# Performance work log

Measured on AMD Instinct MI355X. Metric: run time of the kernel, lower is better.

Reference implementation:

```python
import jax, jax.numpy as jnp
import numpy as np

B, T, N_EMBD = 4, 2048, 1024
NUM_EXPERTS, TOP_K = 8, 2
N_CITIES = 4
LIN = N_EMBD + 32 + N_EMBD // 4 + N_EMBD // 4 + N_EMBD // 8 + N_EMBD // 8  # 1824


def setup_inputs() -> dict:
    key = jax.random.key(0)
    ks = jax.random.split(key, 12)
    s = 0.02  # init std as in _init_weights
    return {
        "x": jax.random.normal(ks[0], (B, T, N_EMBD), jnp.float32),
        "delta_t_info": jax.random.normal(ks[1], (B, T, N_EMBD // 4), jnp.float32),
        "delta_dis_info": jax.random.normal(ks[2], (B, T, N_EMBD // 4), jnp.float32),
        "delta_rg_info": jax.random.normal(ks[3], (B, T, N_EMBD // 8), jnp.float32),
        "delta_entropy_info": jax.random.normal(ks[4], (B, T, N_EMBD // 8), jnp.float32),
        "city_embeddings": jax.random.normal(ks[5], (N_CITIES, 32), jnp.float32),
        "Wg": jax.random.normal(ks[6], (LIN, NUM_EXPERTS), jnp.float32) * s,
        "bg": jnp.zeros((NUM_EXPERTS,), jnp.float32),
        "W1": jax.random.normal(ks[7], (NUM_EXPERTS, N_EMBD, 4 * N_EMBD), jnp.float32) * s,
        "b1": jnp.zeros((NUM_EXPERTS, 4 * N_EMBD), jnp.float32),
        "W2": jax.random.normal(ks[8], (NUM_EXPERTS, 4 * N_EMBD, N_EMBD), jnp.float32) * s,
        "b2": jnp.zeros((NUM_EXPERTS, N_EMBD), jnp.float32),
        "city_index": 1,
    }


def _moe(x, dt, dd, drg, de, city_embeddings, Wg, bg, W1, b1, W2, b2, city_index):
    b, t, _ = x.shape
    city = jnp.broadcast_to(city_embeddings[city_index], (b, t, 32))
    feats = jnp.concatenate([x, city, dt, dd, drg, de], axis=-1)  # [B,T,LIN]
    logits = jnp.einsum("btl,le->bte", feats, Wg) + bg            # eval mode: no noise
    gate1 = jax.nn.softmax(logits, axis=-1)
    _, topi = jax.lax.top_k(logits, TOP_K)                        # [B,T,k]
    # mask of top-k experts per token; scatter(-inf elsewhere) + softmax
    mask = jax.nn.one_hot(topi, NUM_EXPERTS, dtype=jnp.float32).sum(axis=-2) > 0
    sparse_logits = jnp.where(mask, logits, -jnp.inf)
    gates = jax.nn.softmax(sparse_logits, axis=-1)                # zeros outside top-k
    out = jnp.zeros_like(x)
    for e in range(NUM_EXPERTS):  # fixed small expert set
        h = jax.nn.gelu(jnp.einsum("btc,ch->bth", x, W1[e]) + b1[e], approximate=True)
        y = jnp.einsum("bth,hc->btc", h, W2[e]) + b2[e]
        out = out + gates[..., e:e + 1] * y  # gate is exactly 0 for non-topk tokens
    return out, gate1


def reference(x, delta_t_info, delta_dis_info, delta_rg_info, delta_entropy_info,
              city_embeddings, Wg, bg, W1, b1, W2, b2, city_index):
    return _moe(x, delta_t_info, delta_dis_info, delta_rg_info, delta_entropy_info,
                city_embeddings, Wg, bg, W1, b1, W2, b2, city_index)
```

## Files before the change

### kernel.cpp

```cpp
#include <hip/hip_runtime.h>
#include <hip/hip_bf16.h>
#include <stdint.h>

#define NTOK 8192
#define DEMB 1024
#define HDIM 4096
#define NEXP 8
#define LINF 1824
#define MAXPAD 18432

typedef __attribute__((ext_vector_type(8))) __bf16 bf16x8;
typedef __attribute__((ext_vector_type(4))) __bf16 bf16x4v;
typedef __attribute__((ext_vector_type(4))) float f32x4;

__device__ __forceinline__ void gload_lds16(const void* g, void* l) {
  __builtin_amdgcn_global_load_lds(
      (const __attribute__((address_space(1))) void*)g,
      (__attribute__((address_space(3))) void*)l, 16, 0, 0);
}

__device__ __forceinline__ float dot4(float4 a, float4 b) {
  return a.x*b.x + a.y*b.y + a.z*b.z + a.w*b.w;
}

__global__ void __launch_bounds__(256) k_logits(
    const float* __restrict__ x, const float* __restrict__ dt,
    const float* __restrict__ dd, const float* __restrict__ drg,
    const float* __restrict__ de, const float* __restrict__ city,
    const float* __restrict__ Wg, const float* __restrict__ bg,
    const int* __restrict__ city_index,
    float* __restrict__ gate1, int* __restrict__ top_i, float2* __restrict__ top_g,
    __bf16* __restrict__ xb)
{
  __shared__ float WgT[NEXP * LINF];
  const int tid = threadIdx.x;
  const float4* Wg4 = (const float4*)Wg;
  for (int i = tid; i < LINF * NEXP / 4; i += 256) {
    float4 v = Wg4[i];
    int e0 = (i & 1) * 4, f = i >> 1;
    WgT[(e0+0)*LINF + f] = v.x; WgT[(e0+1)*LINF + f] = v.y;
    WgT[(e0+2)*LINF + f] = v.z; WgT[(e0+3)*LINF + f] = v.w;
  }
  __syncthreads();

  const int wave = tid >> 6, lane = tid & 63;
  const int ci = city_index[0];
  const float4* city4 = (const float4*)(city + ci*32);
  const float4 z4 = {0.f, 0.f, 0.f, 0.f};

  #pragma unroll
  for (int k = 0; k < 4; ++k) {
    const int t = blockIdx.x*16 + wave*4 + k;
    const float4* x4 = (const float4*)x + (size_t)t*256;
    float4 xv0 = x4[lane], xv1 = x4[64+lane], xv2 = x4[128+lane], xv3 = x4[192+lane];

    {
      bf16x4v* xrow = (bf16x4v*)(xb + (size_t)t*1024);
      bf16x4v o0, o1, o2, o3;
      o0[0]=(__bf16)xv0.x; o0[1]=(__bf16)xv0.y; o0[2]=(__bf16)xv0.z; o0[3]=(__bf16)xv0.w;
      o1[0]=(__bf16)xv1.x; o1[1]=(__bf16)xv1.y; o1[2]=(__bf16)xv1.z; o1[3]=(__bf16)xv1.w;
      o2[0]=(__bf16)xv2.x; o2[1]=(__bf16)xv2.y; o2[2]=(__bf16)xv2.z; o2[3]=(__bf16)xv2.w;
      o3[0]=(__bf16)xv3.x; o3[1]=(__bf16)xv3.y; o3[2]=(__bf16)xv3.z; o3[3]=(__bf16)xv3.w;
      xrow[lane] = o0; xrow[64+lane] = o1; xrow[128+lane] = o2; xrow[192+lane] = o3;
    }

    float4 cv = (lane < 8) ? city4[lane] : z4;
    float4 tv = ((const float4*)dt)[(size_t)t*64 + lane];
    float4 dv = ((const float4*)dd)[(size_t)t*64 + lane];
    float4 rv = z4, ev = z4;
    if (lane < 32) {
      rv = ((const float4*)drg)[(size_t)t*32 + lane];
      ev = ((const float4*)de )[(size_t)t*32 + lane];
    }
    float a[8];
    const int l8 = lane & 7, l32 = lane & 31;
    #pragma unroll
    for (int e = 0; e < 8; ++e) {
      const float4* W = (const float4*)(WgT + e*LINF);
      float s = dot4(xv0, W[lane]) + dot4(xv1, W[64+lane])
              + dot4(xv2, W[128+lane]) + dot4(xv3, W[192+lane]);
      s += dot4(cv, W[256 + l8]);
      s += dot4(tv, W[264 + lane]) + dot4(dv, W[328 + lane]);
      s += dot4(rv, W[392 + l32]) + dot4(ev, W[424 + l32]);
      a[e] = s;
    }
    #pragma unroll
    for (int off = 32; off > 0; off >>= 1)
      #pragma unroll
      for (int e = 0; e < 8; ++e) a[e] += __shfl_xor(a[e], off);

    float lg[8];
    #pragma unroll
    for (int e = 0; e < 8; ++e) lg[e] = a[e] + bg[e];
    float mx = lg[0];
    #pragma unroll
    for (int e = 1; e < 8; ++e) mx = fmaxf(mx, lg[e]);
    float ex[8]; float s = 0.f;
    #pragma unroll
    for (int e = 0; e < 8; ++e) { ex[e] = expf(lg[e] - mx); s += ex[e]; }
    int i1 = 0; float l1 = lg[0];
    #pragma unroll
    for (int e = 1; e < 8; ++e) if (lg[e] > l1) { l1 = lg[e]; i1 = e; }
    int i2 = -1; float l2 = -1e30f;
    #pragma unroll
    for (int e = 0; e < 8; ++e) if (e != i1 && lg[e] > l2) { l2 = lg[e]; i2 = e; }
    float e2 = expf(l2 - l1);

    if (lane == 0) {
      float inv = 1.f / s;
      float4 o0 = { ex[0]*inv, ex[1]*inv, ex[2]*inv, ex[3]*inv };
      float4 o1 = { ex[4]*inv, ex[5]*inv, ex[6]*inv, ex[7]*inv };
      float4* gp = (float4*)(gate1 + (size_t)t*8);
      gp[0] = o0; gp[1] = o1;
      top_i[t] = i1 | (i2 << 4);
      float2 g = { 1.f / (1.f + e2), e2 / (1.f + e2) };
      top_g[t] = g;
    }
  }
}

__global__ void __launch_bounds__(256) k_build(
    const int* __restrict__ top_i, const float2* __restrict__ top_g,
    int* __restrict__ counts, int* __restrict__ ex_tok, float* __restrict__ ex_gate,
    int2* __restrict__ ppos)
{
  __shared__ int lcnt[8], lbase[8];
  const int tid = threadIdx.x;
  if (tid < 8) lcnt[tid] = 0;
  __syncthreads();
  const int t = blockIdx.x*256 + tid;
  const int ti = top_i[t];
  const int i1 = ti & 15, i2 = ti >> 4;
  const float2 g = top_g[t];
  int p1 = atomicAdd(&lcnt[i1], 1);
  int p2 = atomicAdd(&lcnt[i2], 1);
  __syncthreads();
  if (tid < 8) lbase[tid] = atomicAdd(&counts[tid], lcnt[tid]);
  __syncthreads();
  int s1 = lbase[i1] + p1; ex_tok[i1*NTOK+s1] = t; ex_gate[i1*NTOK+s1] = g.x;
  int s2 = lbase[i2] + p2; ex_tok[i2*NTOK+s2] = t; ex_gate[i2*NTOK+s2] = g.y;
  int2 pp = { i1 | (s1 << 3), i2 | (s2 << 3) };
  ppos[t] = pp;
}

__global__ void k_finalize(const int* __restrict__ counts, int* __restrict__ seg) {
  if (threadIdx.x == 0 && blockIdx.x == 0) {
    int s = 0;
    for (int e = 0; e < 8; ++e) { seg[e] = s; s += (counts[e] + 255) & ~255; }
    seg[8] = s;
  }
}

template<int RDIM, int CDIM>
__global__ void __launch_bounds__(256) k_tconv(
    const float* __restrict__ W, __bf16* __restrict__ WT)
{
  const int e  = blockIdx.z;
  const int c0 = blockIdx.x * 64, r0 = blockIdx.y * 64;
  __shared__ float tb[64 * 65];
  const float* src = W  + (size_t)e * RDIM * CDIM + (size_t)r0 * CDIM + c0;
  __bf16*      dst = WT + (size_t)e * RDIM * CDIM + (size_t)c0 * RDIM + r0;
  const int tx = threadIdx.x & 15, ty = threadIdx.x >> 4;
  #pragma unroll
  for (int i = 0; i < 4; ++i) {
    int r = ty + i*16;
    float4 v = *(const float4*)(src + (size_t)r*CDIM + tx*4);
    tb[(tx*4+0)*65 + r] = v.x; tb[(tx*4+1)*65 + r] = v.y;
    tb[(tx*4+2)*65 + r] = v.z; tb[(tx*4+3)*65 + r] = v.w;
  }
  __syncthreads();
  const int sg = threadIdx.x & 7, dr8 = threadIdx.x >> 3;
  #pragma unroll
  for (int i = 0; i < 2; ++i) {
    int d = dr8 + i*32;
    const float* row = tb + d*65 + sg*8;
    bf16x8 o;
    #pragma unroll
    for (int j = 0; j < 8; ++j) o[j] = (__bf16)row[j];
    *(bf16x8*)(dst + (size_t)d*RDIM + sg*8) = o;
  }
}

template<int KDIM, int KFULL, int NDIM, bool G1>
__global__ void __launch_bounds__(512, 2) k_moe_gemm8(
    const __bf16* __restrict__ Abase, const __bf16* __restrict__ WT,
    const float* __restrict__ bias,
    const int* __restrict__ seg, const int* __restrict__ counts,
    const int* __restrict__ ex_tok,
    int chunk0, __bf16* __restrict__ dstbuf)
{
  constexpr int NT = KDIM / 64;
  const int nx = gridDim.x, ny = gridDim.y, nz = gridDim.z;
  const int total = nx * ny * nz;
  int flat;
  if (G1) flat = blockIdx.x + nx * blockIdx.y;
  else    flat = blockIdx.y + ny * (blockIdx.x + nx * blockIdx.z);
  { int q = total >> 3, r = total & 7; int xcd = flat & 7, idx = flat >> 3;
    flat = (xcd < r ? xcd*(q+1) : r*(q+1) + (xcd-r)*q) + idx; }
  int bx, by, bz;
  if (G1) { bx = flat % nx; by = flat / nx; bz = 0; }
  else    { by = flat % ny; int f2 = flat / ny; bx = f2 % nx; bz = f2 / nx; }

  const int segtot = seg[8];
  const int row0 = chunk0 + bx * 256;
  if (row0 >= segtot) return;
  int e = 0;
  #pragma unroll
  for (int qq = 1; qq < 8; ++qq) if (row0 >= seg[qq]) e = qq;
  const int cnt = counts[e], sege = seg[e];
  const int n0 = by * 256;
  const int kbase = bz * KDIM;

  __shared__ __align__(16) char smem[131072];

  const int tid = threadIdx.x;
  const int wid = tid >> 6, lane = tid & 63;
  const int wm = wid >> 2, wn = wid & 3;
  const int l15 = lane & 15, l4 = lane >> 4;
  const __bf16* Bsrc = WT + (size_t)e * NDIM * KFULL;

  float bv[4];
  if (G1) {
    #pragma unroll
    for (int N = 0; N < 4; ++N)
      bv[N] = bias[(size_t)e*NDIM + n0 + wn*64 + N*16 + l15];
    asm volatile("" :: "v"(bv[0]), "v"(bv[1]), "v"(bv[2]), "v"(bv[3]));
  }

  const __bf16* sp[4][2];
  #pragma unroll
  for (int j = 0; j < 2; ++j) {
    int g = j*512 + tid;
    int sl = g >> 3;
    int kb = (g & 7) ^ (sl & 7);
    #pragma unroll
    for (int mh = 0; mh < 2; ++mh) {
      int wms = (sl >> 6) & 1, rs = sl & 63;
      int R = wms*128 + mh*64 + rs;
      int arow;
      if (G1) { int lr = row0 + R - sege; arow = (lr < cnt) ? ex_tok[e*NTOK + lr] : 0; }
      else    { arow = row0 + R - chunk0; }
      sp[mh][j] = Abase + (size_t)arow * KFULL + kbase + kb*8;
    }
    #pragma unroll
    for (int nh = 0; nh < 2; ++nh) {
      int wns = (sl >> 5) & 3, rs = sl & 31;
      int C = wns*64 + nh*32 + rs;
      sp[2+nh][j] = Bsrc + (size_t)(n0 + C) * KFULL + kbase + kb*8;
    }
  }

  int xo[2];
  #pragma unroll
  for (int kk = 0; kk < 2; ++kk) xo[kk] = (((kk*4 + l4) ^ (l15 & 7)) * 16);
  int arb[4], brb[2];
  #pragma unroll
  for (int m = 0; m < 4; ++m) arb[m] = (wm*64 + m*16 + l15) * 128;
  #pragma unroll
  for (int n = 0; n < 2; ++n) brb[n] = 32768 + (wn*32 + n*16 + l15) * 128;

  auto ISSUE = [&](int h, int tt) {
    char* b = smem + (tt & 1) * 65536 + h * 16384;
    gload_lds16(sp[h][0] + tt*64, b + tid*16);
    gload_lds16(sp[h][1] + tt*64, b + 8192 + tid*16);
  };

  f32x4 acc[8][4] = {};

  ISSUE(0,0); ISSUE(2,0); ISSUE(3,0); ISSUE(1,0);
  ISSUE(0,1); ISSUE(2,1); ISSUE(3,1);
  asm volatile("s_waitcnt vmcnt(10)" ::: "memory");
  __builtin_amdgcn_s_barrier();

  for (int t = 0; t < NT; ++t) {
    const char* cb = smem + (t & 1) * 65536;
    const int tc1 = (t+1 < NT) ? t+1 : NT-1;
    const int tc2 = (t+2 < NT) ? t+2 : NT-1;
    bf16x8 af[4][2], bfr[2][2][2];

    #pragma unroll
    for (int m = 0; m < 4; ++m)
      #pragma unroll
      for (int kk = 0; kk < 2; ++kk)
        af[m][kk] = *(const bf16x8*)(cb + arb[m] + xo[kk]);
    #pragma unroll
    for (int n = 0; n < 2; ++n)
      #pragma unroll
      for (int kk = 0; kk < 2; ++kk)
        bfr[0][n][kk] = *(const bf16x8*)(cb + brb[n] + xo[kk]);
    ISSUE(1, tc1);
    __builtin_amdgcn_s_barrier();
    asm volatile("s_waitcnt lgkmcnt(0)" ::: "memory");
    __builtin_amdgcn_sched_barrier(0);
    __builtin_amdgcn_s_setprio(1);
    #pragma unroll
    for (int m = 0; m < 4; ++m)
      #pragma unroll
      for (int n = 0; n < 2; ++n)
        #pragma unroll
        for (int kk = 0; kk < 2; ++kk)
          acc[m][n] = __builtin_amdgcn_mfma_f32_16x16x32_bf16(af[m][kk], bfr[0][n][kk], acc[m][n], 0, 0, 0);
    __builtin_amdgcn_s_setprio(0);
    asm volatile("s_waitcnt vmcnt(10)" ::: "memory");
    __builtin_amdgcn_s_barrier();

    #pragma unroll
    for (int n = 0; n < 2; ++n)
      #pragma unroll
      for (int kk = 0; kk < 2; ++kk)
        bfr[1][n][kk] = *(const bf16x8*)(cb + 16384 + brb[n] + xo[kk]);
    ISSUE(0, tc2);
    __builtin_amdgcn_s_barrier();
    asm volatile("s_waitcnt lgkmcnt(0)" ::: "memory");
    __builtin_amdgcn_sched_barrier(0);
    __builtin_amdgcn_s_setprio(1);
    #pragma unroll
    for (int m = 0; m < 4; ++m)
      #pragma unroll
      for (int n = 0; n < 2; ++n)
        #pragma unroll
        for (int kk = 0; kk < 2; ++kk)
          acc[m][2+n] = __builtin_amdgcn_mfma_f32_16x16x32_bf16(af[m][kk], bfr[1][n][kk], acc[m][2+n], 0, 0, 0);
    __builtin_amdgcn_s_setprio(0);
    asm volatile("s_waitcnt vmcnt(10)" ::: "memory");
    __builtin_amdgcn_s_barrier();

    #pragma unroll
    for (int m = 0; m < 4; ++m)
      #pragma unroll
      for (int kk = 0; kk < 2; ++kk)
        af[m][kk] = *(const bf16x8*)(cb + 16384 + arb[m] + xo[kk]);
    ISSUE(2, tc2);
    __builtin_amdgcn_s_barrier();
    asm volatile("s_waitcnt lgkmcnt(0)" ::: "memory");
    __builtin_amdgcn_sched_barrier(0);
    __builtin_amdgcn_s_setprio(1);
    #pragma unroll
    for (int m = 0; m < 4; ++m)
      #pragma unroll
      for (int n = 0; n < 2; ++n)
        #pragma unroll
        for (int kk = 0; kk < 2; ++kk)
          acc[4+m][n] = __builtin_amdgcn_mfma_f32_16x16x32_bf16(af[m][kk], bfr[0][n][kk], acc[4+m][n], 0, 0, 0);
    __builtin_amdgcn_s_setprio(0);
    asm volatile("s_waitcnt vmcnt(10)" ::: "memory");
    __builtin_amdgcn_s_barrier();

    ISSUE(3, tc2);
    __builtin_amdgcn_s_barrier();
    __builtin_amdgcn_s_setprio(1);
    #pragma unroll
    for (int m = 0; m < 4; ++m)
      #pragma unroll
      for (int n = 0; n < 2; ++n)
        #pragma unroll
        for (int kk = 0; kk < 2; ++kk)
          acc[4+m][2+n] = __builtin_amdgcn_mfma_f32_16x16x32_bf16(af[m][kk], bfr[1][n][kk], acc[4+m][2+n], 0, 0, 0);
    __builtin_amdgcn_s_setprio(0);
    asm volatile("s_waitcnt vmcnt(10)" ::: "memory");
    __builtin_amdgcn_s_barrier();
  }

  __syncthreads();
  __bf16* Cl = (__bf16*)smem;
  #pragma unroll
  for (int M = 0; M < 8; ++M) {
    #pragma unroll
    for (int N = 0; N < 4; ++N) {
      #pragma unroll
      for (int r2 = 0; r2 < 4; ++r2) {
        float v = acc[M][N][r2];
        if (G1) {
          v += bv[N];
          float z = 2.302208f * (v + 0.044715f * v * v * v);
          v = v / (1.f + exp2f(-z));
        }
        Cl[(wm*128 + M*16 + l4*4 + r2)*256 + wn*64 + N*16 + l15] = (__bf16)v;
      }
    }
  }
  __syncthreads();
  const int drow0 = G1 ? (row0 - chunk0) : row0;
  __bf16* dst = dstbuf + (G1 ? (size_t)0 : (size_t)bz * MAXPAD * NDIM);
  #pragma unroll
  for (int it = 0; it < 16; ++it) {
    int idx2 = it*512 + tid;
    int rr = idx2 >> 5, c8 = (idx2 & 31) * 8;
    *(bf16x8*)(dst + (size_t)(drow0 + rr)*NDIM + n0 + c8) =
        *(const bf16x8*)(Cl + rr*256 + c8);
  }
}

__global__ void __launch_bounds__(256) k_combine(
    const __bf16* __restrict__ pbuf, const int2* __restrict__ ppos,
    const float2* __restrict__ top_g, const int* __restrict__ seg,
    const float* __restrict__ b2, float* __restrict__ out)
{
  const int t = blockIdx.x, tid = threadIdx.x;
  const int2 pp = ppos[t];
  const float2 g = top_g[t];
  const int e1 = pp.x & 7, i1 = pp.x >> 3;
  const int e2 = pp.y & 7, i2 = pp.y >> 3;
  const size_t r1 = (size_t)(seg[e1] + i1) * DEMB;
  const size_t r2 = (size_t)(seg[e2] + i2) * DEMB;
  const __bf16* p0 = pbuf;
  const __bf16* p1 = pbuf + (size_t)MAXPAD * DEMB;
  const int c = tid * 4;
  bf16x4v a0 = *(const bf16x4v*)(p0 + r1 + c);
  bf16x4v a1 = *(const bf16x4v*)(p1 + r1 + c);
  bf16x4v c0 = *(const bf16x4v*)(p0 + r2 + c);
  bf16x4v c1 = *(const bf16x4v*)(p1 + r2 + c);
  float4 ba = *(const float4*)(b2 + (size_t)e1*DEMB + c);
  float4 bb = *(const float4*)(b2 + (size_t)e2*DEMB + c);
  float4 o;
  o.x = g.x*((float)a0[0]+(float)a1[0]+ba.x) + g.y*((float)c0[0]+(float)c1[0]+bb.x);
  o.y = g.x*((float)a0[1]+(float)a1[1]+ba.y) + g.y*((float)c0[1]+(float)c1[1]+bb.y);
  o.z = g.x*((float)a0[2]+(float)a1[2]+ba.z) + g.y*((float)c0[2]+(float)c1[2]+bb.z);
  o.w = g.x*((float)a0[3]+(float)a1[3]+ba.w) + g.y*((float)c0[3]+(float)c1[3]+bb.w);
  *(float4*)(out + (size_t)t*DEMB + c) = o;
}

extern "C" void kernel_launch(void* const* d_in, const int* in_sizes, int n_in,
                              void* d_out, int out_size, void* d_ws, size_t ws_size,
                              hipStream_t stream)
{
  const float* x   = (const float*)d_in[0];
  const float* dt  = (const float*)d_in[1];
  const float* dd  = (const float*)d_in[2];
  const float* drg = (const float*)d_in[3];
  const float* de  = (const float*)d_in[4];
  const float* city= (const float*)d_in[5];
  const float* Wg  = (const float*)d_in[6];
  const float* bg  = (const float*)d_in[7];
  const float* W1  = (const float*)d_in[8];
  const float* b1  = (const float*)d_in[9];
  const float* W2  = (const float*)d_in[10];
  const float* b2  = (const float*)d_in[11];
  const int* city_index = (const int*)d_in[12];

  float* out   = (float*)d_out;
  float* gate1 = out + (size_t)NTOK * DEMB;

  char* p = (char*)d_ws;
  int*    counts  = (int*)p;      p += 256;
  int*    seg     = (int*)p;      p += 256;
  int*    top_i   = (int*)p;      p += (size_t)NTOK*4;
  float2* top_g   = (float2*)p;   p += (size_t)NTOK*8;
  int2*   ppos    = (int2*)p;     p += (size_t)NTOK*8;
  int*    ex_tok  = (int*)p;      p += (size_t)NTOK*NEXP*4;
  float*  ex_gate = (float*)p;    p += (size_t)NTOK*NEXP*4;
  __bf16* xb      = (__bf16*)p;   p += (size_t)NTOK*DEMB*2;
  __bf16* W1T     = (__bf16*)p;   p += (size_t)NEXP*DEMB*HDIM*2;
  __bf16* W2T     = (__bf16*)p;   p += (size_t)NEXP*DEMB*HDIM*2;
  __bf16* pbuf    = (__bf16*)p;   p += (size_t)2*MAXPAD*DEMB*2;
  __bf16* hbuf    = (__bf16*)p;

  size_t fixed = (size_t)(p - (char*)d_ws);
  int CH = MAXPAD;
  while (CH > 0 && fixed + (size_t)CH * HDIM * 2 > ws_size) CH -= 256;
  if (CH <= 0) return;
  int nch = (MAXPAD + CH - 1) / CH;

  (void)hipMemsetAsync(counts, 0, 64, stream);

  k_tconv<DEMB, HDIM><<<dim3(HDIM/64, DEMB/64, NEXP), 256, 0, stream>>>(W1, W1T);
  k_tconv<HDIM, DEMB><<<dim3(DEMB/64, HDIM/64, NEXP), 256, 0, stream>>>(W2, W2T);

  k_logits<<<NTOK/16, 256, 0, stream>>>(x, dt, dd, drg, de, city, Wg, bg,
                                        city_index, gate1, top_i, top_g, xb);
  k_build<<<NTOK/256, 256, 0, stream>>>(top_i, top_g, counts, ex_tok, ex_gate, ppos);
  k_finalize<<<1, 64, 0, stream>>>(counts, seg);

  for (int c = 0; c < nch; ++c) {
    k_moe_gemm8<1024, 1024, HDIM, true><<<dim3(CH/256, HDIM/256, 1), 512, 0, stream>>>(
        xb, W1T, b1, seg, counts, ex_tok, c*CH, hbuf);
    k_moe_gemm8<2048, 4096, DEMB, false><<<dim3(CH/256, DEMB/256, 2), 512, 0, stream>>>(
        hbuf, W2T, b2, seg, counts, ex_tok, c*CH, pbuf);
  }
  k_combine<<<NTOK, 256, 0, stream>>>(pbuf, ppos, top_g, seg, b2, out);
}
```

Before: 519.2 us.

## Switch MoE GEMM to 32x32x16 MFMA and raise second-GEMM split-K to four

The grouped GEMM inner loop now uses 32x32x16 bf16 MFMA tiles in place of 16x16x32, with a new fragment addressing, swizzle and epilogue row mapping. This reduces LDS fragment loads per MFMA and the instruction count. The explicit lgkmcnt waits and sched barriers before each MFMA block are dropped, leaving the compiler to place the waits. The down-projection GEMM splits K four ways instead of two, which increases grid parallelism but doubles partial-buffer traffic and the reads the combine kernel must do.

```diff
diff --git a/kernel.cpp b/kernel.cpp
--- a/kernel.cpp
+++ b/kernel.cpp
@@ -12,6 +12,7 @@
 typedef __attribute__((ext_vector_type(8))) __bf16 bf16x8;
 typedef __attribute__((ext_vector_type(4))) __bf16 bf16x4v;
 typedef __attribute__((ext_vector_type(4))) float f32x4;
+typedef __attribute__((ext_vector_type(16))) float f32x16;
 
 __device__ __forceinline__ void gload_lds16(const void* g, void* l) {
   __builtin_amdgcn_global_load_lds(
@@ -216,15 +217,15 @@
   const int tid = threadIdx.x;
   const int wid = tid >> 6, lane = tid & 63;
   const int wm = wid >> 2, wn = wid & 3;
-  const int l15 = lane & 15, l4 = lane >> 4;
+  const int l31 = lane & 31, l5 = lane >> 5;
   const __bf16* Bsrc = WT + (size_t)e * NDIM * KFULL;
 
-  float bv[4];
+  float bv[2];
   if (G1) {
     #pragma unroll
-    for (int N = 0; N < 4; ++N)
-      bv[N] = bias[(size_t)e*NDIM + n0 + wn*64 + N*16 + l15];
-    asm volatile("" :: "v"(bv[0]), "v"(bv[1]), "v"(bv[2]), "v"(bv[3]));
+    for (int N = 0; N < 2; ++N)
+      bv[N] = bias[(size_t)e*NDIM + n0 + wn*64 + N*32 + l31];
+    asm volatile("" :: "v"(bv[0]), "v"(bv[1]));
   }
 
   const __bf16* sp[4][2];
@@ -250,14 +251,13 @@
     }
   }
 
-  int xo[2];
-  #pragma unroll
-  for (int kk = 0; kk < 2; ++kk) xo[kk] = (((kk*4 + l4) ^ (l15 & 7)) * 16);
-  int arb[4], brb[2];
-  #pragma unroll
-  for (int m = 0; m < 4; ++m) arb[m] = (wm*64 + m*16 + l15) * 128;
-  #pragma unroll
-  for (int n = 0; n < 2; ++n) brb[n] = 32768 + (wn*32 + n*16 + l15) * 128;
+  int xoK[4];
+  #pragma unroll
+  for (int s = 0; s < 4; ++s) xoK[s] = (((s*2 + l5) ^ (lane & 7)) * 16);
+  int aM[2], bN;
+  #pragma unroll
+  for (int M = 0; M < 2; ++M) aM[M] = (wm*64 + M*32 + l31) * 128;
+  bN = 32768 + (wn*32 + l31) * 128;
 
   auto ISSUE = [&](int h, int tt) {
     char* b = smem + (tt & 1) * 65536 + h * 16384;
@@ -265,7 +265,7 @@
     gload_lds16(sp[h][1] + tt*64, b + 8192 + tid*16);
   };
 
-  f32x4 acc[8][4] = {};
+  f32x16 acc[4][2] = {};
 
   ISSUE(0,0); ISSUE(2,0); ISSUE(3,0); ISSUE(1,0);
   ISSUE(0,1); ISSUE(2,1); ISSUE(3,1);
@@ -276,72 +276,56 @@
     const char* cb = smem + (t & 1) * 65536;
     const int tc1 = (t+1 < NT) ? t+1 : NT-1;
     const int tc2 = (t+2 < NT) ? t+2 : NT-1;
-    bf16x8 af[4][2], bfr[2][2][2];
-
-    #pragma unroll
-    for (int m = 0; m < 4; ++m)
-      #pragma unroll
-      for (int kk = 0; kk < 2; ++kk)
-        af[m][kk] = *(const bf16x8*)(cb + arb[m] + xo[kk]);
-    #pragma unroll
-    for (int n = 0; n < 2; ++n)
-      #pragma unroll
-      for (int kk = 0; kk < 2; ++kk)
-        bfr[0][n][kk] = *(const bf16x8*)(cb + brb[n] + xo[kk]);
+    bf16x8 af[2][4], bf0[4], bf1[4];
+
+    #pragma unroll
+    for (int M = 0; M < 2; ++M)
+      #pragma unroll
+      for (int s = 0; s < 4; ++s)
+        af[M][s] = *(const bf16x8*)(cb + aM[M] + xoK[s]);
+    #pragma unroll
+    for (int s = 0; s < 4; ++s)
+      bf0[s] = *(const bf16x8*)(cb + bN + xoK[s]);
     ISSUE(1, tc1);
     __builtin_amdgcn_s_barrier();
-    asm volatile("s_waitcnt lgkmcnt(0)" ::: "memory");
-    __builtin_amdgcn_sched_barrier(0);
     __builtin_amdgcn_s_setprio(1);
     #pragma unroll
-    for (int m = 0; m < 4; ++m)
-      #pragma unroll
-      for (int n = 0; n < 2; ++n)
-        #pragma unroll
-        for (int kk = 0; kk < 2; ++kk)
-          acc[m][n] = __builtin_amdgcn_mfma_f32_16x16x32_bf16(af[m][kk], bfr[0][n][kk], acc[m][n], 0, 0, 0);
+    for (int s = 0; s < 4; ++s)
+      #pragma unroll
+      for (int M = 0; M < 2; ++M)
+        acc[M][0] = __builtin_amdgcn_mfma_f32_32x32x16_bf16(af[M][s], bf0[s], acc[M][0], 0, 0, 0);
     __builtin_amdgcn_s_setprio(0);
     asm volatile("s_waitcnt vmcnt(10)" ::: "memory");
     __builtin_amdgcn_s_barrier();
 
     #pragma unroll
-    for (int n = 0; n < 2; ++n)
-      #pragma unroll
-      for (int kk = 0; kk < 2; ++kk)
-        bfr[1][n][kk] = *(const bf16x8*)(cb + 16384 + brb[n] + xo[kk]);
+    for (int s = 0; s < 4; ++s)
+      bf1[s] = *(const bf16x8*)(cb + 16384 + bN + xoK[s]);
     ISSUE(0, tc2);
     __builtin_amdgcn_s_barrier();
-    asm volatile("s_waitcnt lgkmcnt(0)" ::: "memory");
-    __builtin_amdgcn_sched_barrier(0);
     __builtin_amdgcn_s_setprio(1);
     #pragma unroll
-    for (int m = 0; m < 4; ++m)
-      #pragma unroll
-      for (int n = 0; n < 2; ++n)
-        #pragma unroll
-        for (int kk = 0; kk < 2; ++kk)
-          acc[m][2+n] = __builtin_amdgcn_mfma_f32_16x16x32_bf16(af[m][kk], bfr[1][n][kk], acc[m][2+n], 0, 0, 0);
+    for (int s = 0; s < 4; ++s)
+      #pragma unroll
+      for (int M = 0; M < 2; ++M)
+        acc[M][1] = __builtin_amdgcn_mfma_f32_32x32x16_bf16(af[M][s], bf1[s], acc[M][1], 0, 0, 0);
     __builtin_amdgcn_s_setprio(0);
     asm volatile("s_waitcnt vmcnt(10)" ::: "memory");
     __builtin_amdgcn_s_barrier();
 
     #pragma unroll
-    for (int m = 0; m < 4; ++m)
-      #pragma unroll
-      for (int kk = 0; kk < 2; ++kk)
-        af[m][kk] = *(const bf16x8*)(cb + 16384 + arb[m] + xo[kk]);
+    for (int M = 0; M < 2; ++M)
+      #pragma unroll
+      for (int s = 0; s < 4; ++s)
+        af[M][s] = *(const bf16x8*)(cb + 16384 + aM[M] + xoK[s]);
     ISSUE(2, tc2);
     __builtin_amdgcn_s_barrier();
-    asm volatile("s_waitcnt lgkmcnt(0)" ::: "memory");
-    __builtin_amdgcn_sched_barrier(0);
     __builtin_amdgcn_s_setprio(1);
     #pragma unroll
-    for (int m = 0; m < 4; ++m)
-      #pragma unroll
-      for (int n = 0; n < 2; ++n)
-        #pragma unroll
-        for (int kk = 0; kk < 2; ++kk)
-          acc[4+m][n] = __builtin_amdgcn_mfma_f32_16x16x32_bf16(af[m][kk], bfr[0][n][kk], acc[4+m][n], 0, 0, 0);
+    for (int s = 0; s < 4; ++s)
+      #pragma unroll
+      for (int M = 0; M < 2; ++M)
+        acc[2+M][0] = __builtin_amdgcn_mfma_f32_32x32x16_bf16(af[M][s], bf0[s], acc[2+M][0], 0, 0, 0);
     __builtin_amdgcn_s_setprio(0);
     asm volatile("s_waitcnt vmcnt(10)" ::: "memory");
     __builtin_amdgcn_s_barrier();
@@ -350,12 +334,10 @@
     __builtin_amdgcn_s_barrier();
     __builtin_amdgcn_s_setprio(1);
     #pragma unroll
-    for (int m = 0; m < 4; ++m)
-      #pragma unroll
-      for (int n = 0; n < 2; ++n)
-        #pragma unroll
-        for (int kk = 0; kk < 2; ++kk)
-          acc[4+m][2+n] = __builtin_amdgcn_mfma_f32_16x16x32_bf16(af[m][kk], bfr[1][n][kk], acc[4+m][2+n], 0, 0, 0);
+    for (int s = 0; s < 4; ++s)
+      #pragma unroll
+      for (int M = 0; M < 2; ++M)
+        acc[2+M][1] = __builtin_amdgcn_mfma_f32_32x32x16_bf16(af[M][s], bf1[s], acc[2+M][1], 0, 0, 0);
     __builtin_amdgcn_s_setprio(0);
     asm volatile("s_waitcnt vmcnt(10)" ::: "memory");
     __builtin_amdgcn_s_barrier();
@@ -364,18 +346,19 @@
   __syncthreads();
   __bf16* Cl = (__bf16*)smem;
   #pragma unroll
-  for (int M = 0; M < 8; ++M) {
-    #pragma unroll
-    for (int N = 0; N < 4; ++N) {
-      #pragma unroll
-      for (int r2 = 0; r2 < 4; ++r2) {
-        float v = acc[M][N][r2];
+  for (int M = 0; M < 4; ++M) {
+    #pragma unroll
+    for (int N = 0; N < 2; ++N) {
+      #pragma unroll
+      for (int r = 0; r < 16; ++r) {
+        float v = acc[M][N][r];
         if (G1) {
           v += bv[N];
           float z = 2.302208f * (v + 0.044715f * v * v * v);
           v = v / (1.f + exp2f(-z));
         }
-        Cl[(wm*128 + M*16 + l4*4 + r2)*256 + wn*64 + N*16 + l15] = (__bf16)v;
+        int row = wm*128 + M*32 + (r & 3) + 8*(r >> 2) + 4*l5;
+        Cl[row*256 + wn*64 + N*32 + l31] = (__bf16)v;
       }
     }
   }
@@ -403,20 +386,24 @@
   const int e2 = pp.y & 7, i2 = pp.y >> 3;
   const size_t r1 = (size_t)(seg[e1] + i1) * DEMB;
   const size_t r2 = (size_t)(seg[e2] + i2) * DEMB;
-  const __bf16* p0 = pbuf;
-  const __bf16* p1 = pbuf + (size_t)MAXPAD * DEMB;
   const int c = tid * 4;
-  bf16x4v a0 = *(const bf16x4v*)(p0 + r1 + c);
-  bf16x4v a1 = *(const bf16x4v*)(p1 + r1 + c);
-  bf16x4v c0 = *(const bf16x4v*)(p0 + r2 + c);
-  bf16x4v c1 = *(const bf16x4v*)(p1 + r2 + c);
   float4 ba = *(const float4*)(b2 + (size_t)e1*DEMB + c);
   float4 bb = *(const float4*)(b2 + (size_t)e2*DEMB + c);
+  float s1x = ba.x, s1y = ba.y, s1z = ba.z, s1w = ba.w;
+  float s2x = bb.x, s2y = bb.y, s2z = bb.z, s2w = bb.w;
+  #pragma unroll
+  for (int p = 0; p < 4; ++p) {
+    const __bf16* pb = pbuf + (size_t)p * MAXPAD * DEMB;
+    bf16x4v a = *(const bf16x4v*)(pb + r1 + c);
+    bf16x4v b = *(const bf16x4v*)(pb + r2 + c);
+    s1x += (float)a[0]; s1y += (float)a[1]; s1z += (float)a[2]; s1w += (float)a[3];
+    s2x += (float)b[0]; s2y += (float)b[1]; s2z += (float)b[2]; s2w += (float)b[3];
+  }
   float4 o;
-  o.x = g.x*((float)a0[0]+(float)a1[0]+ba.x) + g.y*((float)c0[0]+(float)c1[0]+bb.x);
-  o.y = g.x*((float)a0[1]+(float)a1[1]+ba.y) + g.y*((float)c0[1]+(float)c1[1]+bb.y);
-  o.z = g.x*((float)a0[2]+(float)a1[2]+ba.z) + g.y*((float)c0[2]+(float)c1[2]+bb.z);
-  o.w = g.x*((float)a0[3]+(float)a1[3]+ba.w) + g.y*((float)c0[3]+(float)c1[3]+bb.w);
+  o.x = g.x*s1x + g.y*s2x;
+  o.y = g.x*s1y + g.y*s2y;
+  o.z = g.x*s1z + g.y*s2z;
+  o.w = g.x*s1w + g.y*s2w;
   *(float4*)(out + (size_t)t*DEMB + c) = o;
 }
 
@@ -452,7 +439,7 @@
   __bf16* xb      = (__bf16*)p;   p += (size_t)NTOK*DEMB*2;
   __bf16* W1T     = (__bf16*)p;   p += (size_t)NEXP*DEMB*HDIM*2;
   __bf16* W2T     = (__bf16*)p;   p += (size_t)NEXP*DEMB*HDIM*2;
-  __bf16* pbuf    = (__bf16*)p;   p += (size_t)2*MAXPAD*DEMB*2;
+  __bf16* pbuf    = (__bf16*)p;   p += (size_t)4*MAXPAD*DEMB*2;
   __bf16* hbuf    = (__bf16*)p;
 
   size_t fixed = (size_t)(p - (char*)d_ws);
@@ -474,7 +461,7 @@
   for (int c = 0; c < nch; ++c) {
     k_moe_gemm8<1024, 1024, HDIM, true><<<dim3(CH/256, HDIM/256, 1), 512, 0, stream>>>(
         xb, W1T, b1, seg, counts, ex_tok, c*CH, hbuf);
-    k_moe_gemm8<2048, 4096, DEMB, false><<<dim3(CH/256, DEMB/256, 2), 512, 0, stream>>>(
+    k_moe_gemm8<1024, 4096, DEMB, false><<<dim3(CH/256, DEMB/256, 4), 512, 0, stream>>>(
         hbuf, W2T, b2, seg, counts, ex_tok, c*CH, pbuf);
   }
   k_combine<<<NTOK, 256, 0, stream>>>(pbuf, ppos, top_g, seg, b2, out);
```

Measured after the change: 573.2 us. 1.1x slower.
